# Optimization experiments

Hardware: AMD Instinct MI355X
Metric: run time of the kernel (lower is better)

## Reference

```python
import jax, jax.numpy as jnp
import numpy as np
from jax import lax

DN = ('NCHW', 'OIHW', 'NCHW')

def conv(x, w, b, stride):
    y = lax.conv_general_dilated(x, w, window_strides=(stride, stride),
                                 padding='VALID', dimension_numbers=DN)
    return y + b[None, :, None, None]

def setup_inputs() -> dict:
    key = jax.random.key(0)
    ks = jax.random.split(key, 7)
    B = 4096
    def he(k, shape, fan_in):
        return jax.random.normal(k, shape, jnp.float32) * np.sqrt(2.0 / fan_in)
    return {
        'x':  jax.random.normal(ks[0], (B, 3, 48, 64), jnp.float32),
        'w1': he(ks[1], (32, 3, 8, 8), 3 * 8 * 8),
        'b1': jnp.zeros((32,), jnp.float32),
        'w2': he(ks[2], (64, 32, 3, 3), 32 * 3 * 3),
        'b2': jnp.zeros((64,), jnp.float32),
        'w3': he(ks[3], (64, 64, 3, 3), 64 * 3 * 3),
        'b3': jnp.zeros((64,), jnp.float32),
        'w4': he(ks[4], (512, 960), 960),
        'b4': jnp.zeros((512,), jnp.float32),
        'w5': he(ks[5], (2, 512), 512),
        'b5': jnp.zeros((2,), jnp.float32),
    }

def reference(x, w1, b1, w2, b2, w3, b3, w4, b4, w5, b5):
    # conv1 (k8 s4): [B,3,48,64] -> [B,32,11,15]
    x1 = conv(x, w1, b1, 4)
    # side reduction (torch code does this on CPU with python loops):
    # sum over batch and channel dims of pre-ReLU activation, divided by 32
    ave1 = jnp.sum(x1, axis=(0, 1)) / 32.0          # [11,15]
    x2 = jax.nn.relu(x1)
    # conv2 (k3 s2): -> [B,64,5,7]
    x3 = conv(x2, w2, b2, 2)
    ave2 = jnp.sum(x3, axis=(0, 1)) / 64.0          # [5,7]
    x4 = jax.nn.relu(x3)
    # conv3 (k3 s1): -> [B,64,3,5]
    x5 = conv(x4, w3, b3, 1)
    ave3 = jnp.sum(x5, axis=(0, 1)) / 64.0          # [3,5]
    x6 = jax.nn.relu(x5)
    # fc head: flatten (C,H,W order, matching torch) -> 960 -> 512 -> 2
    h = x6.reshape(x6.shape[0], -1)                 # [B,960]
    h = jax.nn.relu(h @ w4.T + b4)
    out = h @ w5.T + b5                             # [B,2]
    return out, ave1, ave2, ave3
```

## Files before the change

### kernel.cpp

```cpp
#include <hip/hip_runtime.h>
#include <hip/hip_bf16.h>

#define BATCH 4096

typedef __attribute__((ext_vector_type(8))) short short8;
typedef __attribute__((ext_vector_type(4))) short short4_t;
typedef __attribute__((ext_vector_type(4))) float f32x4;

#define MFMA_BF16 __builtin_amdgcn_mfma_f32_16x16x32_bf16

__device__ __forceinline__ float frelu(float v) { return v > 0.f ? v : 0.f; }
__device__ __forceinline__ unsigned short f2bf(float f) {
    return __builtin_bit_cast(unsigned short, __float2bfloat16(f));
}
__device__ __forceinline__ short8 cvt8(const float* p) {
    float4 a = *(const float4*)p;
    float4 b = *(const float4*)(p + 4);
    short8 r;
    r[0] = (short)f2bf(a.x); r[1] = (short)f2bf(a.y); r[2] = (short)f2bf(a.z); r[3] = (short)f2bf(a.w);
    r[4] = (short)f2bf(b.x); r[5] = (short)f2bf(b.y); r[6] = (short)f2bf(b.z); r[7] = (short)f2bf(b.w);
    return r;
}

__global__ __launch_bounds__(256) void prep_kernel(const float* __restrict__ w2, const float* __restrict__ w3,
                                                   const float* __restrict__ w4, const float* __restrict__ b5,
                                                   unsigned short* __restrict__ w2p, unsigned short* __restrict__ w3p,
                                                   unsigned short* __restrict__ w4p, float* __restrict__ out) {
    int idx = blockIdx.x * 256 + threadIdx.x;
    if (idx < 18432) {
        int oc = idx / 288, k = idx % 288;
        int khw = k / 32, ic = k % 32;
        w2p[idx] = f2bf(w2[oc * 288 + ic * 9 + khw]);
    } else if (idx < 55296) {
        int j = idx - 18432;
        int oc = j / 576, k = j % 576;
        int khw = k / 64, ic = k % 64;
        w3p[j] = f2bf(w3[oc * 576 + ic * 9 + khw]);
    } else if (idx < 546816) {
        int j = idx - 55296;
        int n = j / 960, k = j % 960;
        int pos = k / 64, oc = k % 64;
        w4p[j] = f2bf(w4[n * 960 + oc * 15 + pos]);
    } else if (idx < 555008) {
        int j = idx - 546816;
        out[j] = b5[j & 1];
    } else if (idx < 555223) {
        out[8192 + (idx - 555008)] = 0.f;
    }
}

__global__ __launch_bounds__(256) void fused_convs(const float* __restrict__ x,
                                                   const float* __restrict__ w1, const float* __restrict__ b1,
                                                   const unsigned short* __restrict__ w2p, const float* __restrict__ b2,
                                                   const unsigned short* __restrict__ w3p, const float* __restrict__ b3,
                                                   unsigned short* __restrict__ x6, float* __restrict__ redbuf) {
    constexpr int RS = 68;
    __shared__ __align__(16) unsigned short xl[3 * 48 * RS];
    __shared__ __align__(16) unsigned short x2l[165 * 36];
    __shared__ float red1l[165];
    __shared__ float red2l[35];
    __shared__ float red3l[15];
    unsigned short* x4l = xl;
    unsigned short* x6l = xl + 2560;

    const int img = blockIdx.x;
    const int tid = threadIdx.x;
    const int wave = tid >> 6, lane = tid & 63;
    const int col = lane & 15, quad = lane >> 4;

    if (tid < 165) red1l[tid] = 0.f;
    else if (tid < 200) red2l[tid - 165] = 0.f;
    else if (tid < 215) red3l[tid - 200] = 0.f;

    {
        const float4* xs = (const float4*)(x + (size_t)img * 9216);
        #pragma unroll
        for (int i = 0; i < 9; ++i) {
            const int idx = tid + i * 256;
            float4 v = xs[idx];
            const int fo = idx * 4;
            const int r = fo >> 6, cf = fo & 63;
            short4_t s;
            s[0] = (short)f2bf(v.x); s[1] = (short)f2bf(v.y);
            s[2] = (short)f2bf(v.z); s[3] = (short)f2bf(v.w);
            *(short4_t*)(xl + r * RS + cf) = s;
        }
    }

    short8 Bf1[2][6];
    #pragma unroll
    for (int nt = 0; nt < 2; ++nt) {
        const int oc = nt * 16 + col;
        #pragma unroll
        for (int c = 0; c < 6; ++c)
            Bf1[nt][c] = cvt8(w1 + oc * 192 + c * 32 + quad * 8);
    }
    const float bias0 = b1[col], bias1 = b1[col + 16];
    __syncthreads();

    #pragma unroll
    for (int ti = 0; ti < 3; ++ti) {
        const int t = wave + ti * 4;
        if (t >= 11) break;
        const int posA = t * 16 + col;
        const int pm = posA < 165 ? posA : 164;
        const int oh = pm / 15, ow = pm % 15;
        f32x4 acc0 = {0.f, 0.f, 0.f, 0.f}, acc1 = {0.f, 0.f, 0.f, 0.f};
        #pragma unroll
        for (int c = 0; c < 6; ++c) {
            const int ic = c >> 1;
            const int kh = (c & 1) * 4 + quad;
            const unsigned short* ap = xl + (ic * 48 + oh * 4 + kh) * RS + ow * 4;
            short8 af;
            *(short4_t*)&af       = *(const short4_t*)ap;
            *((short4_t*)&af + 1) = *(const short4_t*)(ap + 4);
            acc0 = MFMA_BF16(af, Bf1[0][c], acc0, 0, 0, 0);
            acc1 = MFMA_BF16(af, Bf1[1][c], acc1, 0, 0, 0);
        }
        #pragma unroll
        for (int r = 0; r < 4; ++r) {
            const int pr = t * 16 + quad * 4 + r;
            float v0 = acc0[r] + bias0;
            float v1 = acc1[r] + bias1;
            float s = v0 + v1;
            s += __shfl_xor(s, 1); s += __shfl_xor(s, 2);
            s += __shfl_xor(s, 4); s += __shfl_xor(s, 8);
            if (pr < 165) {
                if (col == 0) atomicAdd(&red1l[pr], s);
                x2l[pr * 36 + col]      = f2bf(frelu(v0));
                x2l[pr * 36 + col + 16] = f2bf(frelu(v1));
            }
        }
    }
    __syncthreads();

    {
        const int oc2 = wave * 16 + col;
        short8 Bf2[9];
        #pragma unroll
        for (int c = 0; c < 9; ++c)
            Bf2[c] = *(const short8*)(w2p + (size_t)oc2 * 288 + c * 32 + quad * 8);
        const float bv2 = b2[oc2];

        int aoff[3];
        #pragma unroll
        for (int mt = 0; mt < 3; ++mt) {
            int p = mt * 16 + col; p = p < 35 ? p : 34;
            const int oh2 = p / 7, ow2 = p % 7;
            aoff[mt] = (oh2 * 30 + ow2 * 2) * 36 + quad * 8;
        }
        f32x4 acc[3] = {};
        #pragma unroll
        for (int c = 0; c < 9; ++c) {
            const int kh = c / 3, kw = c % 3;
            const int koff = (kh * 15 + kw) * 36;
            #pragma unroll
            for (int mt = 0; mt < 3; ++mt) {
                const unsigned short* ap = x2l + aoff[mt] + koff;
                short8 af;
                *(short4_t*)&af       = *(const short4_t*)ap;
                *((short4_t*)&af + 1) = *(const short4_t*)(ap + 4);
                acc[mt] = MFMA_BF16(af, Bf2[c], acc[mt], 0, 0, 0);
            }
        }
        #pragma unroll
        for (int mt = 0; mt < 3; ++mt) {
            #pragma unroll
            for (int r = 0; r < 4; ++r) {
                const int pr = mt * 16 + quad * 4 + r;
                float v = acc[mt][r] + bv2;
                float s = v;
                s += __shfl_xor(s, 1); s += __shfl_xor(s, 2);
                s += __shfl_xor(s, 4); s += __shfl_xor(s, 8);
                if (pr < 35) {
                    x4l[pr * 72 + oc2] = f2bf(frelu(v));
                    if (col == 0) atomicAdd(&red2l[pr], s);
                }
            }
        }
    }
    __syncthreads();

    {
        const int oc3 = wave * 16 + col;
        short8 Bf3[18];
        #pragma unroll
        for (int c = 0; c < 18; ++c)
            Bf3[c] = *(const short8*)(w3p + (size_t)oc3 * 576 + c * 32 + quad * 8);
        const float bv3 = b3[oc3];

        int p = col < 15 ? col : 14;
        const int abase = ((p / 5) * 7 + (p % 5)) * 72;
        f32x4 acc = {};
        #pragma unroll
        for (int c = 0; c < 18; ++c) {
            const int khw = c >> 1, kh = khw / 3, kw = khw % 3;
            const unsigned short* ap = x4l + abase + (kh * 7 + kw) * 72 + (c & 1) * 32 + quad * 8;
            short8 af = *(const short8*)ap;
            acc = MFMA_BF16(af, Bf3[c], acc, 0, 0, 0);
        }
        #pragma unroll
        for (int r = 0; r < 4; ++r) {
            const int pr = quad * 4 + r;
            float v = acc[r] + bv3;
            float s = v;
            s += __shfl_xor(s, 1); s += __shfl_xor(s, 2);
            s += __shfl_xor(s, 4); s += __shfl_xor(s, 8);
            if (pr < 15) {
                x6l[pr * 64 + oc3] = f2bf(frelu(v));
                if (col == 0) atomicAdd(&red3l[pr], s);
            }
        }
    }
    __syncthreads();

    if (tid < 120) ((float4*)(x6 + (size_t)img * 960))[tid] = ((const float4*)x6l)[tid];
    if (tid < 215) {
        float v = tid < 165 ? red1l[tid] : (tid < 200 ? red2l[tid - 165] : red3l[tid - 200]);
        redbuf[(size_t)tid * 4096 + img] = v;
    }
}

__global__ __launch_bounds__(256) void reduce_aves(const float* __restrict__ redbuf, float* __restrict__ out) {
    const int row = blockIdx.x;
    float s = 0.f;
    for (int i = threadIdx.x; i < 4096; i += 256) s += redbuf[(size_t)row * 4096 + i];
    s += __shfl_down(s, 32); s += __shfl_down(s, 16); s += __shfl_down(s, 8);
    s += __shfl_down(s, 4);  s += __shfl_down(s, 2);  s += __shfl_down(s, 1);
    __shared__ float wsum[4];
    if ((threadIdx.x & 63) == 0) wsum[threadIdx.x >> 6] = s;
    __syncthreads();
    if (threadIdx.x == 0)
        out[8192 + row] = (wsum[0] + wsum[1] + wsum[2] + wsum[3]) * (row < 165 ? 0.03125f : 0.015625f);
}

__global__ __launch_bounds__(256) void fc45_mfma(const unsigned short* __restrict__ x6,
                                                 const unsigned short* __restrict__ w4p, const float* __restrict__ b4,
                                                 const float* __restrict__ w5, float* __restrict__ out) {
    __shared__ float outl[32][2];
    const int tid = threadIdx.x;
    const int wave = tid >> 6, lane = tid & 63;
    const int col = lane & 15, quad = lane >> 4;
    if (tid < 64) outl[tid >> 1][tid & 1] = 0.f;
    const int m0 = blockIdx.x * 32;
    const int oc = blockIdx.y * 64 + wave * 16 + col;

    const unsigned short* brow  = w4p + (size_t)oc * 960 + quad * 8;
    const unsigned short* arow0 = x6 + (size_t)(m0 + col) * 960 + quad * 8;
    const unsigned short* arow1 = arow0 + 16 * 960;
    f32x4 acc0 = {}, acc1 = {};
    __syncthreads();
    #pragma unroll 6
    for (int c = 0; c < 30; ++c) {
        short8 Bf = *(const short8*)(brow + c * 32);
        short8 a0 = *(const short8*)(arow0 + c * 32);
        short8 a1 = *(const short8*)(arow1 + c * 32);
        acc0 = MFMA_BF16(a0, Bf, acc0, 0, 0, 0);
        acc1 = MFMA_BF16(a1, Bf, acc1, 0, 0, 0);
    }
    const float bb = b4[oc], u0 = w5[oc], u1 = w5[512 + oc];
    #pragma unroll
    for (int mi = 0; mi < 2; ++mi) {
        const f32x4 acc = mi ? acc1 : acc0;
        #pragma unroll
        for (int r = 0; r < 4; ++r) {
            float h = frelu(acc[r] + bb);
            float l0 = h * u0, l1 = h * u1;
            l0 += __shfl_xor(l0, 1); l0 += __shfl_xor(l0, 2); l0 += __shfl_xor(l0, 4); l0 += __shfl_xor(l0, 8);
            l1 += __shfl_xor(l1, 1); l1 += __shfl_xor(l1, 2); l1 += __shfl_xor(l1, 4); l1 += __shfl_xor(l1, 8);
            if (col == 0) {
                atomicAdd(&outl[mi * 16 + quad * 4 + r][0], l0);
                atomicAdd(&outl[mi * 16 + quad * 4 + r][1], l1);
            }
        }
    }
    __syncthreads();
    if (tid < 64) atomicAdd(&out[(m0 + (tid >> 1)) * 2 + (tid & 1)], outl[tid >> 1][tid & 1]);
}

extern "C" void kernel_launch(void* const* d_in, const int* in_sizes, int n_in,
                              void* d_out, int out_size, void* d_ws, size_t ws_size,
                              hipStream_t stream) {
    const float* x  = (const float*)d_in[0];
    const float* w1 = (const float*)d_in[1];
    const float* b1 = (const float*)d_in[2];
    const float* w2 = (const float*)d_in[3];
    const float* b2 = (const float*)d_in[4];
    const float* w3 = (const float*)d_in[5];
    const float* b3 = (const float*)d_in[6];
    const float* w4 = (const float*)d_in[7];
    const float* b4 = (const float*)d_in[8];
    const float* w5 = (const float*)d_in[9];
    const float* b5 = (const float*)d_in[10];
    float* out = (float*)d_out;

    unsigned short* ws = (unsigned short*)d_ws;
    unsigned short* x6  = ws;
    unsigned short* w2p = ws + 3932160;
    unsigned short* w3p = ws + 3950592;
    unsigned short* w4p = ws + 3987456;
    float* redbuf = (float*)((char*)d_ws + 8957952);

    prep_kernel<<<2169, 256, 0, stream>>>(w2, w3, w4, b5, w2p, w3p, w4p, out);
    fused_convs<<<BATCH, 256, 0, stream>>>(x, w1, b1, w2p, b2, w3p, b3, x6, redbuf);
    reduce_aves<<<215, 256, 0, stream>>>(redbuf, out);
    fc45_mfma<<<dim3(128, 8), 256, 0, stream>>>(x6, w4p, b4, w5, out);
}
```

Measured before the change: 347.5 us.

## Cut register and LDS use in fused conv kernel to raise occupancy

Converts w1 to bf16 in the prep kernel and streams weight fragments from global/L2 per MFMA instead of preloading them into registers. It also aliases all stage buffers in one LDS region and adds launch_bounds(256,8). A barrier is added so conv1 results can overwrite the input tile, conv3 uses two accumulators for ILP, and the reduction buffer is transposed to be image-major for coalesced writes. The trade is more repeated weight loads and an extra sync in exchange for more resident blocks per CU.

Result: no change. 349.2 us (+0.5%).

```diff
diff --git a/kernel.cpp b/kernel.cpp
--- a/kernel.cpp
+++ b/kernel.cpp
@@ -13,64 +13,57 @@
 __device__ __forceinline__ unsigned short f2bf(float f) {
     return __builtin_bit_cast(unsigned short, __float2bfloat16(f));
 }
-__device__ __forceinline__ short8 cvt8(const float* p) {
-    float4 a = *(const float4*)p;
-    float4 b = *(const float4*)(p + 4);
-    short8 r;
-    r[0] = (short)f2bf(a.x); r[1] = (short)f2bf(a.y); r[2] = (short)f2bf(a.z); r[3] = (short)f2bf(a.w);
-    r[4] = (short)f2bf(b.x); r[5] = (short)f2bf(b.y); r[6] = (short)f2bf(b.z); r[7] = (short)f2bf(b.w);
-    return r;
-}
-
-__global__ __launch_bounds__(256) void prep_kernel(const float* __restrict__ w2, const float* __restrict__ w3,
-                                                   const float* __restrict__ w4, const float* __restrict__ b5,
-                                                   unsigned short* __restrict__ w2p, unsigned short* __restrict__ w3p,
-                                                   unsigned short* __restrict__ w4p, float* __restrict__ out) {
+
+__global__ __launch_bounds__(256) void prep_kernel(const float* __restrict__ w1, const float* __restrict__ w2,
+                                                   const float* __restrict__ w3, const float* __restrict__ w4,
+                                                   const float* __restrict__ b5,
+                                                   unsigned short* __restrict__ w1p, unsigned short* __restrict__ w2p,
+                                                   unsigned short* __restrict__ w3p, unsigned short* __restrict__ w4p,
+                                                   float* __restrict__ out) {
     int idx = blockIdx.x * 256 + threadIdx.x;
-    if (idx < 18432) {
-        int oc = idx / 288, k = idx % 288;
+    if (idx < 6144) {
+        w1p[idx] = f2bf(w1[idx]);
+    } else if (idx < 24576) {
+        int j = idx - 6144;
+        int oc = j / 288, k = j % 288;
         int khw = k / 32, ic = k % 32;
-        w2p[idx] = f2bf(w2[oc * 288 + ic * 9 + khw]);
-    } else if (idx < 55296) {
-        int j = idx - 18432;
+        w2p[j] = f2bf(w2[oc * 288 + ic * 9 + khw]);
+    } else if (idx < 61440) {
+        int j = idx - 24576;
         int oc = j / 576, k = j % 576;
         int khw = k / 64, ic = k % 64;
         w3p[j] = f2bf(w3[oc * 576 + ic * 9 + khw]);
-    } else if (idx < 546816) {
-        int j = idx - 55296;
+    } else if (idx < 552960) {
+        int j = idx - 61440;
         int n = j / 960, k = j % 960;
         int pos = k / 64, oc = k % 64;
         w4p[j] = f2bf(w4[n * 960 + oc * 15 + pos]);
-    } else if (idx < 555008) {
-        int j = idx - 546816;
+    } else if (idx < 561152) {
+        int j = idx - 552960;
         out[j] = b5[j & 1];
-    } else if (idx < 555223) {
-        out[8192 + (idx - 555008)] = 0.f;
-    }
-}
-
-__global__ __launch_bounds__(256) void fused_convs(const float* __restrict__ x,
-                                                   const float* __restrict__ w1, const float* __restrict__ b1,
-                                                   const unsigned short* __restrict__ w2p, const float* __restrict__ b2,
-                                                   const unsigned short* __restrict__ w3p, const float* __restrict__ b3,
-                                                   unsigned short* __restrict__ x6, float* __restrict__ redbuf) {
+    } else if (idx < 561367) {
+        out[8192 + (idx - 561152)] = 0.f;
+    }
+}
+
+__global__ __launch_bounds__(256, 8) void fused_convs(const float* __restrict__ x,
+                                                      const unsigned short* __restrict__ w1p, const float* __restrict__ b1,
+                                                      const unsigned short* __restrict__ w2p, const float* __restrict__ b2,
+                                                      const unsigned short* __restrict__ w3p, const float* __restrict__ b3,
+                                                      unsigned short* __restrict__ x6, float* __restrict__ redbuf) {
     constexpr int RS = 68;
-    __shared__ __align__(16) unsigned short xl[3 * 48 * RS];
-    __shared__ __align__(16) unsigned short x2l[165 * 36];
-    __shared__ float red1l[165];
-    __shared__ float red2l[35];
-    __shared__ float red3l[15];
-    unsigned short* x4l = xl;
-    unsigned short* x6l = xl + 2560;
+    __shared__ __align__(16) unsigned short ub[3 * 48 * RS];
+    __shared__ float red[215];
+    unsigned short* x2l = ub;
+    unsigned short* x4l = ub + 5952;
+    unsigned short* x6l = ub + 8480;
 
     const int img = blockIdx.x;
     const int tid = threadIdx.x;
     const int wave = tid >> 6, lane = tid & 63;
     const int col = lane & 15, quad = lane >> 4;
 
-    if (tid < 165) red1l[tid] = 0.f;
-    else if (tid < 200) red2l[tid - 165] = 0.f;
-    else if (tid < 215) red3l[tid - 200] = 0.f;
+    if (tid < 215) red[tid] = 0.f;
 
     {
         const float4* xs = (const float4*)(x + (size_t)img * 9216);
@@ -83,21 +76,15 @@
             short4_t s;
             s[0] = (short)f2bf(v.x); s[1] = (short)f2bf(v.y);
             s[2] = (short)f2bf(v.z); s[3] = (short)f2bf(v.w);
-            *(short4_t*)(xl + r * RS + cf) = s;
-        }
-    }
-
-    short8 Bf1[2][6];
-    #pragma unroll
-    for (int nt = 0; nt < 2; ++nt) {
-        const int oc = nt * 16 + col;
-        #pragma unroll
-        for (int c = 0; c < 6; ++c)
-            Bf1[nt][c] = cvt8(w1 + oc * 192 + c * 32 + quad * 8);
+            *(short4_t*)(ub + r * RS + cf) = s;
+        }
     }
     const float bias0 = b1[col], bias1 = b1[col + 16];
     __syncthreads();
 
+    f32x4 c1a[3][2] = {};
+    const unsigned short* w1b0 = w1p + (size_t)col * 192 + quad * 8;
+    const unsigned short* w1b1 = w1b0 + 16 * 192;
     #pragma unroll
     for (int ti = 0; ti < 3; ++ti) {
         const int t = wave + ti * 4;
@@ -105,28 +92,36 @@
         const int posA = t * 16 + col;
         const int pm = posA < 165 ? posA : 164;
         const int oh = pm / 15, ow = pm % 15;
-        f32x4 acc0 = {0.f, 0.f, 0.f, 0.f}, acc1 = {0.f, 0.f, 0.f, 0.f};
         #pragma unroll
         for (int c = 0; c < 6; ++c) {
             const int ic = c >> 1;
             const int kh = (c & 1) * 4 + quad;
-            const unsigned short* ap = xl + (ic * 48 + oh * 4 + kh) * RS + ow * 4;
+            const unsigned short* ap = ub + (ic * 48 + oh * 4 + kh) * RS + ow * 4;
             short8 af;
             *(short4_t*)&af       = *(const short4_t*)ap;
             *((short4_t*)&af + 1) = *(const short4_t*)(ap + 4);
-            acc0 = MFMA_BF16(af, Bf1[0][c], acc0, 0, 0, 0);
-            acc1 = MFMA_BF16(af, Bf1[1][c], acc1, 0, 0, 0);
-        }
+            short8 B0 = *(const short8*)(w1b0 + c * 32);
+            short8 B1 = *(const short8*)(w1b1 + c * 32);
+            c1a[ti][0] = MFMA_BF16(af, B0, c1a[ti][0], 0, 0, 0);
+            c1a[ti][1] = MFMA_BF16(af, B1, c1a[ti][1], 0, 0, 0);
+        }
+    }
+    __syncthreads();
+
+    #pragma unroll
+    for (int ti = 0; ti < 3; ++ti) {
+        const int t = wave + ti * 4;
+        if (t >= 11) break;
         #pragma unroll
         for (int r = 0; r < 4; ++r) {
             const int pr = t * 16 + quad * 4 + r;
-            float v0 = acc0[r] + bias0;
-            float v1 = acc1[r] + bias1;
+            float v0 = c1a[ti][0][r] + bias0;
+            float v1 = c1a[ti][1][r] + bias1;
             float s = v0 + v1;
             s += __shfl_xor(s, 1); s += __shfl_xor(s, 2);
             s += __shfl_xor(s, 4); s += __shfl_xor(s, 8);
             if (pr < 165) {
-                if (col == 0) atomicAdd(&red1l[pr], s);
+                if (col == 0) atomicAdd(&red[pr], s);
                 x2l[pr * 36 + col]      = f2bf(frelu(v0));
                 x2l[pr * 36 + col + 16] = f2bf(frelu(v1));
             }
@@ -136,45 +131,40 @@
 
     {
         const int oc2 = wave * 16 + col;
-        short8 Bf2[9];
-        #pragma unroll
-        for (int c = 0; c < 9; ++c)
-            Bf2[c] = *(const short8*)(w2p + (size_t)oc2 * 288 + c * 32 + quad * 8);
-        const float bv2 = b2[oc2];
-
+        const unsigned short* w2b = w2p + (size_t)oc2 * 288 + quad * 8;
         int aoff[3];
         #pragma unroll
         for (int mt = 0; mt < 3; ++mt) {
             int p = mt * 16 + col; p = p < 35 ? p : 34;
-            const int oh2 = p / 7, ow2 = p % 7;
-            aoff[mt] = (oh2 * 30 + ow2 * 2) * 36 + quad * 8;
-        }
-        f32x4 acc[3] = {};
+            aoff[mt] = ((p / 7) * 30 + (p % 7) * 2) * 36 + quad * 8;
+        }
+        f32x4 a2[3] = {};
         #pragma unroll
         for (int c = 0; c < 9; ++c) {
-            const int kh = c / 3, kw = c % 3;
-            const int koff = (kh * 15 + kw) * 36;
+            short8 Bc = *(const short8*)(w2b + c * 32);
+            const int koff = ((c / 3) * 15 + (c % 3)) * 36;
             #pragma unroll
             for (int mt = 0; mt < 3; ++mt) {
                 const unsigned short* ap = x2l + aoff[mt] + koff;
                 short8 af;
                 *(short4_t*)&af       = *(const short4_t*)ap;
                 *((short4_t*)&af + 1) = *(const short4_t*)(ap + 4);
-                acc[mt] = MFMA_BF16(af, Bf2[c], acc[mt], 0, 0, 0);
-            }
-        }
+                a2[mt] = MFMA_BF16(af, Bc, a2[mt], 0, 0, 0);
+            }
+        }
+        const float bv2 = b2[oc2];
         #pragma unroll
         for (int mt = 0; mt < 3; ++mt) {
             #pragma unroll
             for (int r = 0; r < 4; ++r) {
                 const int pr = mt * 16 + quad * 4 + r;
-                float v = acc[mt][r] + bv2;
+                float v = a2[mt][r] + bv2;
                 float s = v;
                 s += __shfl_xor(s, 1); s += __shfl_xor(s, 2);
                 s += __shfl_xor(s, 4); s += __shfl_xor(s, 8);
                 if (pr < 35) {
                     x4l[pr * 72 + oc2] = f2bf(frelu(v));
-                    if (col == 0) atomicAdd(&red2l[pr], s);
+                    if (col == 0) atomicAdd(&red[165 + pr], s);
                 }
             }
         }
@@ -183,48 +173,46 @@
 
     {
         const int oc3 = wave * 16 + col;
-        short8 Bf3[18];
-        #pragma unroll
-        for (int c = 0; c < 18; ++c)
-            Bf3[c] = *(const short8*)(w3p + (size_t)oc3 * 576 + c * 32 + quad * 8);
-        const float bv3 = b3[oc3];
-
+        const unsigned short* w3b = w3p + (size_t)oc3 * 576 + quad * 8;
         int p = col < 15 ? col : 14;
         const int abase = ((p / 5) * 7 + (p % 5)) * 72;
-        f32x4 acc = {};
-        #pragma unroll
-        for (int c = 0; c < 18; ++c) {
-            const int khw = c >> 1, kh = khw / 3, kw = khw % 3;
-            const unsigned short* ap = x4l + abase + (kh * 7 + kw) * 72 + (c & 1) * 32 + quad * 8;
-            short8 af = *(const short8*)ap;
-            acc = MFMA_BF16(af, Bf3[c], acc, 0, 0, 0);
-        }
+        f32x4 aA = {}, aB = {};
+        #pragma unroll
+        for (int cc = 0; cc < 9; ++cc) {
+            const int kh = cc / 3, kw = cc % 3;
+            const unsigned short* bp = x4l + abase + (kh * 7 + kw) * 72 + quad * 8;
+            short8 af0 = *(const short8*)bp;
+            short8 af1 = *(const short8*)(bp + 32);
+            short8 B0 = *(const short8*)(w3b + (2 * cc) * 32);
+            short8 B1 = *(const short8*)(w3b + (2 * cc + 1) * 32);
+            aA = MFMA_BF16(af0, B0, aA, 0, 0, 0);
+            aB = MFMA_BF16(af1, B1, aB, 0, 0, 0);
+        }
+        f32x4 a3 = aA + aB;
+        const float bv3 = b3[oc3];
         #pragma unroll
         for (int r = 0; r < 4; ++r) {
             const int pr = quad * 4 + r;
-            float v = acc[r] + bv3;
+            float v = a3[r] + bv3;
             float s = v;
             s += __shfl_xor(s, 1); s += __shfl_xor(s, 2);
             s += __shfl_xor(s, 4); s += __shfl_xor(s, 8);
             if (pr < 15) {
                 x6l[pr * 64 + oc3] = f2bf(frelu(v));
-                if (col == 0) atomicAdd(&red3l[pr], s);
+                if (col == 0) atomicAdd(&red[200 + pr], s);
             }
         }
     }
     __syncthreads();
 
     if (tid < 120) ((float4*)(x6 + (size_t)img * 960))[tid] = ((const float4*)x6l)[tid];
-    if (tid < 215) {
-        float v = tid < 165 ? red1l[tid] : (tid < 200 ? red2l[tid - 165] : red3l[tid - 200]);
-        redbuf[(size_t)tid * 4096 + img] = v;
-    }
+    if (tid < 215) redbuf[(size_t)img * 216 + tid] = red[tid];
 }
 
 __global__ __launch_bounds__(256) void reduce_aves(const float* __restrict__ redbuf, float* __restrict__ out) {
     const int row = blockIdx.x;
     float s = 0.f;
-    for (int i = threadIdx.x; i < 4096; i += 256) s += redbuf[(size_t)row * 4096 + i];
+    for (int i = threadIdx.x; i < 4096; i += 256) s += redbuf[(size_t)i * 216 + row];
     s += __shfl_down(s, 32); s += __shfl_down(s, 16); s += __shfl_down(s, 8);
     s += __shfl_down(s, 4);  s += __shfl_down(s, 2);  s += __shfl_down(s, 1);
     __shared__ float wsum[4];
@@ -296,13 +284,14 @@
 
     unsigned short* ws = (unsigned short*)d_ws;
     unsigned short* x6  = ws;
-    unsigned short* w2p = ws + 3932160;
-    unsigned short* w3p = ws + 3950592;
-    unsigned short* w4p = ws + 3987456;
-    float* redbuf = (float*)((char*)d_ws + 8957952);
-
-    prep_kernel<<<2169, 256, 0, stream>>>(w2, w3, w4, b5, w2p, w3p, w4p, out);
-    fused_convs<<<BATCH, 256, 0, stream>>>(x, w1, b1, w2p, b2, w3p, b3, x6, redbuf);
+    unsigned short* w1p = ws + 3932160;
+    unsigned short* w2p = ws + 3938304;
+    unsigned short* w3p = ws + 3956736;
+    unsigned short* w4p = ws + 3993600;
+    float* redbuf = (float*)((char*)d_ws + 8970240);
+
+    prep_kernel<<<2193, 256, 0, stream>>>(w1, w2, w3, w4, b5, w1p, w2p, w3p, w4p, out);
+    fused_convs<<<BATCH, 256, 0, stream>>>(x, w1p, b1, w2p, b2, w3p, b3, x6, redbuf);
     reduce_aves<<<215, 256, 0, stream>>>(redbuf, out);
     fc45_mfma<<<dim3(128, 8), 256, 0, stream>>>(x6, w4p, b4, w5, out);
 }
```
